# Performance work log

Hardware: AMD Instinct MI355X
Metric: run time of the kernel (lower is better)

The kernel has to match this reference:

```python
import jax, jax.numpy as jnp
import numpy as np

EPS = 1e-12


def setup_inputs() -> dict:
    key = jax.random.key(0)
    k1, k2 = jax.random.split(key)
    ide_feats = jax.random.normal(k1, (4096, 256), dtype=jnp.float32)
    u_feats = jax.random.normal(k2, (16384, 256), dtype=jnp.float32)
    return {"ide_feats": ide_feats, "u_feats": u_feats}


def reference(ide_feats, u_feats):
    # euclidean_dist: sqrt(sum((x_i - y_j)^2) + eps) -> [N, M]
    # computed via the GEMM expansion to avoid the [N, M, D] intermediate
    x2 = jnp.sum(ide_feats * ide_feats, axis=-1)[:, None]   # [N, 1]
    y2 = jnp.sum(u_feats * u_feats, axis=-1)[None, :]       # [1, M]
    xy = jnp.einsum('nd,md->nm', ide_feats, u_feats)        # [N, M]
    d2 = jnp.maximum(x2 + y2 - 2.0 * xy, 0.0)
    dists = jnp.sqrt(d2 + EPS)                              # [N, M]
    d = jnp.mean(dists, axis=-1)                            # [N]
    # dist_loss: sum_{i,j} sqrt((d_i - d_j)^2 + eps)
    diff = d[:, None] - d[None, :]                          # [N, N]
    loss = jnp.sum(jnp.sqrt(diff * diff + EPS))
    return loss
```

## Files before the change

kernel.cpp:

```cpp
#include <hip/hip_runtime.h>
#include <hip/hip_bf16.h>
#include <cstdint>

#define N_IDE 4096
#define M_U   16384
#define D_DIM 256
#define EPSF  1e-12f
#define INV_M (1.0f / 16384.0f)

typedef _Float16 f16x8 __attribute__((ext_vector_type(8)));
typedef float    f32x4 __attribute__((ext_vector_type(4)));

__device__ __forceinline__ void gll16(const void* g, void* l) {
  __builtin_amdgcn_global_load_lds(
      (const __attribute__((address_space(1))) void*)(uintptr_t)g,
      (__attribute__((address_space(3))) void*)(uint32_t)(uintptr_t)l,
      16, 0, 0);
}

__device__ __forceinline__ unsigned short f2h_bits(float f) {
  _Float16 h = (_Float16)f;
  return __builtin_bit_cast(unsigned short, h);
}

#define SBAR()  asm volatile("s_barrier" ::: "memory")

__global__ __launch_bounds__(256) void k_conv(const float* __restrict__ ide,
                                              const float* __restrict__ u,
                                              unsigned short* __restrict__ Ah,
                                              unsigned short* __restrict__ Bh,
                                              float* __restrict__ x2,
                                              float* __restrict__ y2) {
  int gw = (blockIdx.x * 256 + threadIdx.x) >> 6;
  int l  = threadIdx.x & 63;
  const float4* src;
  ushort4* dst;
  float* nrm;
  if (gw < N_IDE) {
    src = (const float4*)(ide + (size_t)gw * D_DIM);
    dst = (ushort4*)(Ah + (size_t)gw * D_DIM);
    nrm = x2 + gw;
  } else {
    int r = gw - N_IDE;
    src = (const float4*)(u + (size_t)r * D_DIM);
    dst = (ushort4*)(Bh + (size_t)r * D_DIM);
    nrm = y2 + r;
  }
  float4 v = src[l];
  float s = v.x * v.x + v.y * v.y + v.z * v.z + v.w * v.w;
  ushort4 o;
  o.x = f2h_bits(v.x); o.y = f2h_bits(v.y);
  o.z = f2h_bits(v.z); o.w = f2h_bits(v.w);
  dst[l] = o;
#pragma unroll
  for (int m = 1; m <= 32; m <<= 1) s += __shfl_xor(s, m, 64);
  if (l == 0) *nrm = s;
}

__global__ __launch_bounds__(512, 2) void k_gemm(const unsigned short* __restrict__ Ah,
                                                 const unsigned short* __restrict__ Bh,
                                                 const float* __restrict__ x2,
                                                 const float* __restrict__ y2,
                                                 float* __restrict__ partial) {
  __shared__ __align__(16) unsigned short sA[2][16384];
  __shared__ __align__(16) unsigned short sB[2][16384];
  __shared__ float rowacc[4][256];

  const int t    = threadIdx.x;
  const int w    = t >> 6;
  const int l    = t & 63;
  const int lrow = l & 15;
  const int lhi  = l >> 4;
  const int wm   = w >> 2, wn = w & 3;
  const int bn   = blockIdx.x;
  const int bm   = blockIdx.y;

  const int sr  = t >> 3;
  const int skc = (t & 7) ^ (sr & 7);
  const size_t soff = (size_t)sr * D_DIM + (size_t)skc * 8;

  const unsigned short* Abase = Ah + (size_t)bm * 256 * D_DIM;
  const unsigned short* Bbase = Bh + (size_t)bn * 256 * D_DIM;

  auto stA = [&](int k1, int h) {
    const unsigned short* src = Abase + (size_t)h * 128 * D_DIM + k1 * 64 + soff;
    unsigned short* dst = &sA[k1 & 1][h * 8192 + w * 512];
    gll16(src, dst);
    gll16(src + 64 * D_DIM, dst + 4096);
  };
  auto stB = [&](int k1, int h) {
    const unsigned short* src = Bbase + (size_t)h * 128 * D_DIM + k1 * 64 + soff;
    unsigned short* dst = &sB[k1 & 1][h * 8192 + w * 512];
    gll16(src, dst);
    gll16(src + 64 * D_DIM, dst + 4096);
  };

  stA(0, 0); stA(0, 1);
  stB(0, 0); stB(0, 1);
  stB(1, 0); stB(1, 1);
  asm volatile("s_waitcnt vmcnt(4)" ::: "memory");
  SBAR();

  const int sl0 = ((lhi)     ^ (lrow & 7)) * 8;
  const int sl1 = ((lhi + 4) ^ (lrow & 7)) * 8;

  f32x4 acc[8][4];
#pragma unroll
  for (int mi = 0; mi < 8; ++mi)
#pragma unroll
    for (int nj = 0; nj < 4; ++nj)
      acc[mi][nj] = (f32x4){0.f, 0.f, 0.f, 0.f};

#pragma unroll
  for (int kt = 0; kt < 4; ++kt) {
    const unsigned short* Ab = &sA[kt & 1][wm * 8192 + lrow * 64];
    const unsigned short* Bb = &sB[kt & 1][(wn >> 1) * 8192 + ((wn & 1) * 64 + lrow) * 64];
    f16x8 bf[4][2], af[4];

#pragma unroll
    for (int nj = 0; nj < 4; ++nj) {
      bf[nj][0] = *(const f16x8*)(Bb + nj * 1024 + sl0);
      bf[nj][1] = *(const f16x8*)(Bb + nj * 1024 + sl1);
    }
#pragma unroll
    for (int mi = 0; mi < 4; ++mi)
      af[mi] = *(const f16x8*)(Ab + mi * 1024 + sl0);
    if (kt < 3) stA(kt + 1, 0);
    SBAR();
    __builtin_amdgcn_s_setprio(1);
#pragma unroll
    for (int mi = 0; mi < 4; ++mi)
#pragma unroll
      for (int nj = 0; nj < 4; ++nj)
        acc[mi][nj] = __builtin_amdgcn_mfma_f32_16x16x32_f16(af[mi], bf[nj][0],
                                                             acc[mi][nj], 0, 0, 0);
    __builtin_amdgcn_s_setprio(0);
    SBAR();

#pragma unroll
    for (int mi = 0; mi < 4; ++mi)
      af[mi] = *(const f16x8*)(Ab + (64 + mi * 16) * 64 + sl0);
    if (kt < 3) stA(kt + 1, 1);
    SBAR();
    __builtin_amdgcn_s_setprio(1);
#pragma unroll
    for (int mi = 0; mi < 4; ++mi)
#pragma unroll
      for (int nj = 0; nj < 4; ++nj)
        acc[4 + mi][nj] = __builtin_amdgcn_mfma_f32_16x16x32_f16(af[mi], bf[nj][0],
                                                                 acc[4 + mi][nj], 0, 0, 0);
    __builtin_amdgcn_s_setprio(0);
    SBAR();

#pragma unroll
    for (int mi = 0; mi < 4; ++mi)
      af[mi] = *(const f16x8*)(Ab + mi * 1024 + sl1);
    if (kt < 2) stB(kt + 2, 0);
    SBAR();
    __builtin_amdgcn_s_setprio(1);
#pragma unroll
    for (int mi = 0; mi < 4; ++mi)
#pragma unroll
      for (int nj = 0; nj < 4; ++nj)
        acc[mi][nj] = __builtin_amdgcn_mfma_f32_16x16x32_f16(af[mi], bf[nj][1],
                                                             acc[mi][nj], 0, 0, 0);
    __builtin_amdgcn_s_setprio(0);
    SBAR();

#pragma unroll
    for (int mi = 0; mi < 4; ++mi)
      af[mi] = *(const f16x8*)(Ab + (64 + mi * 16) * 64 + sl1);
    if (kt < 2) stB(kt + 2, 1);
    SBAR();
    __builtin_amdgcn_s_setprio(1);
#pragma unroll
    for (int mi = 0; mi < 4; ++mi)
#pragma unroll
      for (int nj = 0; nj < 4; ++nj)
        acc[4 + mi][nj] = __builtin_amdgcn_mfma_f32_16x16x32_f16(af[mi], bf[nj][1],
                                                                 acc[4 + mi][nj], 0, 0, 0);
    __builtin_amdgcn_s_setprio(0);
    if (kt < 2)       asm volatile("s_waitcnt vmcnt(4)" ::: "memory");
    else if (kt == 2) asm volatile("s_waitcnt vmcnt(0)" ::: "memory");
    SBAR();
  }

  float yv[4];
#pragma unroll
  for (int nj = 0; nj < 4; ++nj)
    yv[nj] = y2[bn * 256 + wn * 64 + nj * 16 + lrow];

#pragma unroll
  for (int mi = 0; mi < 8; ++mi) {
    float4 x2v = *(const float4*)&x2[bm * 256 + wm * 128 + mi * 16 + lhi * 4];
    float xr[4] = {x2v.x, x2v.y, x2v.z, x2v.w};
    float rv[4];
#pragma unroll
    for (int rr = 0; rr < 4; ++rr) {
      float ssum = 0.f;
#pragma unroll
      for (int nj = 0; nj < 4; ++nj) {
        float d2 = xr[rr] + yv[nj] - 2.0f * acc[mi][nj][rr];
        d2 = fmaxf(d2, 0.0f);
        ssum += __builtin_amdgcn_sqrtf(d2 + EPSF);
      }
      ssum += __shfl_xor(ssum, 1, 64);
      ssum += __shfl_xor(ssum, 2, 64);
      ssum += __shfl_xor(ssum, 4, 64);
      ssum += __shfl_xor(ssum, 8, 64);
      rv[rr] = ssum;
    }
    if (lrow == 0)
      *(float4*)&rowacc[wn][wm * 128 + mi * 16 + lhi * 4] =
          make_float4(rv[0], rv[1], rv[2], rv[3]);
  }

  __syncthreads();
  if (t < 256)
    partial[(size_t)bn * N_IDE + bm * 256 + t] =
        rowacc[0][t] + rowacc[1][t] + rowacc[2][t] + rowacc[3][t];
}

__global__ __launch_bounds__(256) void k_dsum(const float* __restrict__ partial,
                                              float* __restrict__ d) {
  int k = blockIdx.x * 256 + threadIdx.x;
  float s = 0.f;
#pragma unroll
  for (int b = 0; b < 64; ++b) s += partial[(size_t)b * N_IDE + k];
  d[k] = s;
}

__global__ __launch_bounds__(256) void k_loss(const float* __restrict__ d,
                                              float* __restrict__ out) {
  __shared__ float sd[N_IDE];
  __shared__ float wsum[4];
  int t = threadIdx.x;
  for (int k = t; k < N_IDE; k += 256) sd[k] = d[k];
  __syncthreads();
  int tid = blockIdx.x * 256 + t;
  int i   = tid >> 4;
  int jl  = tid & 15;
  float di = sd[i];
  float s  = 0.f;
  for (int k = 0; k < 256; ++k) {
    float diff = (di - sd[jl + k * 16]) * INV_M;
    s += __builtin_amdgcn_sqrtf(diff * diff + EPSF);
  }
#pragma unroll
  for (int m = 1; m <= 32; m <<= 1) s += __shfl_xor(s, m, 64);
  if ((t & 63) == 0) wsum[t >> 6] = s;
  __syncthreads();
  if (t == 0) atomicAdd(out, wsum[0] + wsum[1] + wsum[2] + wsum[3]);
}

extern "C" void kernel_launch(void* const* d_in, const int* in_sizes, int n_in,
                              void* d_out, int out_size, void* d_ws, size_t ws_size,
                              hipStream_t stream) {
  (void)in_sizes; (void)n_in; (void)out_size; (void)ws_size;
  const float* ide = (const float*)d_in[0];
  const float* u   = (const float*)d_in[1];
  float* out = (float*)d_out;

  char* ws = (char*)d_ws;
  size_t off = 0;
  unsigned short* Ah = (unsigned short*)(ws + off); off += (size_t)N_IDE * D_DIM * 2;
  unsigned short* Bh = (unsigned short*)(ws + off); off += (size_t)M_U  * D_DIM * 2;
  float* x2      = (float*)(ws + off); off += (size_t)N_IDE * 4;
  float* y2      = (float*)(ws + off); off += (size_t)M_U * 4;
  float* partial = (float*)(ws + off); off += (size_t)64 * N_IDE * 4;
  float* dvec    = (float*)(ws + off); off += (size_t)N_IDE * 4;

  hipMemsetAsync(d_out, 0, sizeof(float), stream);
  k_conv<<<(N_IDE + M_U) / 4, 256, 0, stream>>>(ide, u, Ah, Bh, x2, y2);
  k_gemm<<<dim3(64, 16), 512, 0, stream>>>(Ah, Bh, x2, y2, partial);
  k_dsum<<<N_IDE / 256, 256, 0, stream>>>(partial, dvec);
  k_loss<<<256, 256, 0, stream>>>(dvec, out);
}
```

Before: 152.0 us.

## Restructure GEMM K-loop pipeline, fold dsum into loss, drop memset

The GEMM main loop is reorganized so that LDS fragments for the next k-tile are register-prefetched while MFMAs run, and the next tile's A and B global-to-LDS loads are issued together once per k-tile instead of staggered two tiles ahead for B. Separately, the d-vector reduction kernel is removed: each k_loss block now sums the 64 partials itself. The hipMemsetAsync of the output is replaced by a store inside k_conv. These changes cut launches and barriers, but every loss block now redundantly reads the full partial buffer, and the shallower B prefetch may expose more load latency.

```diff
diff --git a/kernel.cpp b/kernel.cpp
--- a/kernel.cpp
+++ b/kernel.cpp
@@ -30,7 +30,9 @@
                                               unsigned short* __restrict__ Ah,
                                               unsigned short* __restrict__ Bh,
                                               float* __restrict__ x2,
-                                              float* __restrict__ y2) {
+                                              float* __restrict__ y2,
+                                              float* __restrict__ out) {
+  if (blockIdx.x == 0 && threadIdx.x == 0) out[0] = 0.f;
   int gw = (blockIdx.x * 256 + threadIdx.x) >> 6;
   int l  = threadIdx.x & 63;
   const float4* src;
@@ -97,12 +99,23 @@
 
   stA(0, 0); stA(0, 1);
   stB(0, 0); stB(0, 1);
-  stB(1, 0); stB(1, 1);
-  asm volatile("s_waitcnt vmcnt(4)" ::: "memory");
+  asm volatile("s_waitcnt vmcnt(0)" ::: "memory");
   SBAR();
 
   const int sl0 = ((lhi)     ^ (lrow & 7)) * 8;
   const int sl1 = ((lhi + 4) ^ (lrow & 7)) * 8;
+
+  f16x8 afA[4], afB[4], bf0[4], bf1[4];
+  {
+    const unsigned short* Ab0 = &sA[0][wm * 8192 + lrow * 64];
+    const unsigned short* Bb0 = &sB[0][(wn >> 1) * 8192 + ((wn & 1) * 64 + lrow) * 64];
+#pragma unroll
+    for (int nj = 0; nj < 4; ++nj)
+      bf0[nj] = *(const f16x8*)(Bb0 + nj * 1024 + sl0);
+#pragma unroll
+    for (int mi = 0; mi < 4; ++mi)
+      afA[mi] = *(const f16x8*)(Ab0 + mi * 1024 + sl0);
+  }
 
   f32x4 acc[8][4];
 #pragma unroll
@@ -115,73 +128,69 @@
   for (int kt = 0; kt < 4; ++kt) {
     const unsigned short* Ab = &sA[kt & 1][wm * 8192 + lrow * 64];
     const unsigned short* Bb = &sB[kt & 1][(wn >> 1) * 8192 + ((wn & 1) * 64 + lrow) * 64];
-    f16x8 bf[4][2], af[4];
-
-#pragma unroll
-    for (int nj = 0; nj < 4; ++nj) {
-      bf[nj][0] = *(const f16x8*)(Bb + nj * 1024 + sl0);
-      bf[nj][1] = *(const f16x8*)(Bb + nj * 1024 + sl1);
+
+    __builtin_amdgcn_s_setprio(1);
+#pragma unroll
+    for (int mi = 0; mi < 4; ++mi)
+#pragma unroll
+      for (int nj = 0; nj < 4; ++nj)
+        acc[mi][nj] = __builtin_amdgcn_mfma_f32_16x16x32_f16(afA[mi], bf0[nj],
+                                                             acc[mi][nj], 0, 0, 0);
+    __builtin_amdgcn_s_setprio(0);
+#pragma unroll
+    for (int mi = 0; mi < 4; ++mi)
+      afB[mi] = *(const f16x8*)(Ab + (64 + mi * 16) * 64 + sl0);
+    if (kt < 3) { stA(kt + 1, 0); stA(kt + 1, 1); stB(kt + 1, 0); stB(kt + 1, 1); }
+    SBAR();
+
+    __builtin_amdgcn_s_setprio(1);
+#pragma unroll
+    for (int mi = 0; mi < 4; ++mi)
+#pragma unroll
+      for (int nj = 0; nj < 4; ++nj)
+        acc[4 + mi][nj] = __builtin_amdgcn_mfma_f32_16x16x32_f16(afB[mi], bf0[nj],
+                                                                 acc[4 + mi][nj], 0, 0, 0);
+    __builtin_amdgcn_s_setprio(0);
+#pragma unroll
+    for (int mi = 0; mi < 4; ++mi)
+      afA[mi] = *(const f16x8*)(Ab + mi * 1024 + sl1);
+#pragma unroll
+    for (int nj = 0; nj < 4; ++nj)
+      bf1[nj] = *(const f16x8*)(Bb + nj * 1024 + sl1);
+    SBAR();
+
+    __builtin_amdgcn_s_setprio(1);
+#pragma unroll
+    for (int mi = 0; mi < 4; ++mi)
+#pragma unroll
+      for (int nj = 0; nj < 4; ++nj)
+        acc[mi][nj] = __builtin_amdgcn_mfma_f32_16x16x32_f16(afA[mi], bf1[nj],
+                                                             acc[mi][nj], 0, 0, 0);
+    __builtin_amdgcn_s_setprio(0);
+#pragma unroll
+    for (int mi = 0; mi < 4; ++mi)
+      afB[mi] = *(const f16x8*)(Ab + (64 + mi * 16) * 64 + sl1);
+    if (kt < 3) asm volatile("s_waitcnt vmcnt(0)" ::: "memory");
+    SBAR();
+
+    __builtin_amdgcn_s_setprio(1);
+#pragma unroll
+    for (int mi = 0; mi < 4; ++mi)
+#pragma unroll
+      for (int nj = 0; nj < 4; ++nj)
+        acc[4 + mi][nj] = __builtin_amdgcn_mfma_f32_16x16x32_f16(afB[mi], bf1[nj],
+                                                                 acc[4 + mi][nj], 0, 0, 0);
+    __builtin_amdgcn_s_setprio(0);
+    if (kt < 3) {
+      const unsigned short* Abn = &sA[(kt + 1) & 1][wm * 8192 + lrow * 64];
+      const unsigned short* Bbn = &sB[(kt + 1) & 1][(wn >> 1) * 8192 + ((wn & 1) * 64 + lrow) * 64];
+#pragma unroll
+      for (int nj = 0; nj < 4; ++nj)
+        bf0[nj] = *(const f16x8*)(Bbn + nj * 1024 + sl0);
+#pragma unroll
+      for (int mi = 0; mi < 4; ++mi)
+        afA[mi] = *(const f16x8*)(Abn + mi * 1024 + sl0);
     }
-#pragma unroll
-    for (int mi = 0; mi < 4; ++mi)
-      af[mi] = *(const f16x8*)(Ab + mi * 1024 + sl0);
-    if (kt < 3) stA(kt + 1, 0);
-    SBAR();
-    __builtin_amdgcn_s_setprio(1);
-#pragma unroll
-    for (int mi = 0; mi < 4; ++mi)
-#pragma unroll
-      for (int nj = 0; nj < 4; ++nj)
-        acc[mi][nj] = __builtin_amdgcn_mfma_f32_16x16x32_f16(af[mi], bf[nj][0],
-                                                             acc[mi][nj], 0, 0, 0);
-    __builtin_amdgcn_s_setprio(0);
-    SBAR();
-
-#pragma unroll
-    for (int mi = 0; mi < 4; ++mi)
-      af[mi] = *(const f16x8*)(Ab + (64 + mi * 16) * 64 + sl0);
-    if (kt < 3) stA(kt + 1, 1);
-    SBAR();
-    __builtin_amdgcn_s_setprio(1);
-#pragma unroll
-    for (int mi = 0; mi < 4; ++mi)
-#pragma unroll
-      for (int nj = 0; nj < 4; ++nj)
-        acc[4 + mi][nj] = __builtin_amdgcn_mfma_f32_16x16x32_f16(af[mi], bf[nj][0],
-                                                                 acc[4 + mi][nj], 0, 0, 0);
-    __builtin_amdgcn_s_setprio(0);
-    SBAR();
-
-#pragma unroll
-    for (int mi = 0; mi < 4; ++mi)
-      af[mi] = *(const f16x8*)(Ab + mi * 1024 + sl1);
-    if (kt < 2) stB(kt + 2, 0);
-    SBAR();
-    __builtin_amdgcn_s_setprio(1);
-#pragma unroll
-    for (int mi = 0; mi < 4; ++mi)
-#pragma unroll
-      for (int nj = 0; nj < 4; ++nj)
-        acc[mi][nj] = __builtin_amdgcn_mfma_f32_16x16x32_f16(af[mi], bf[nj][1],
-                                                             acc[mi][nj], 0, 0, 0);
-    __builtin_amdgcn_s_setprio(0);
-    SBAR();
-
-#pragma unroll
-    for (int mi = 0; mi < 4; ++mi)
-      af[mi] = *(const f16x8*)(Ab + (64 + mi * 16) * 64 + sl1);
-    if (kt < 2) stB(kt + 2, 1);
-    SBAR();
-    __builtin_amdgcn_s_setprio(1);
-#pragma unroll
-    for (int mi = 0; mi < 4; ++mi)
-#pragma unroll
-      for (int nj = 0; nj < 4; ++nj)
-        acc[4 + mi][nj] = __builtin_amdgcn_mfma_f32_16x16x32_f16(af[mi], bf[nj][1],
-                                                                 acc[4 + mi][nj], 0, 0, 0);
-    __builtin_amdgcn_s_setprio(0);
-    if (kt < 2)       asm volatile("s_waitcnt vmcnt(4)" ::: "memory");
-    else if (kt == 2) asm volatile("s_waitcnt vmcnt(0)" ::: "memory");
     SBAR();
   }
 
@@ -221,21 +230,17 @@
         rowacc[0][t] + rowacc[1][t] + rowacc[2][t] + rowacc[3][t];
 }
 
-__global__ __launch_bounds__(256) void k_dsum(const float* __restrict__ partial,
-                                              float* __restrict__ d) {
-  int k = blockIdx.x * 256 + threadIdx.x;
-  float s = 0.f;
-#pragma unroll
-  for (int b = 0; b < 64; ++b) s += partial[(size_t)b * N_IDE + k];
-  d[k] = s;
-}
-
-__global__ __launch_bounds__(256) void k_loss(const float* __restrict__ d,
+__global__ __launch_bounds__(256) void k_loss(const float* __restrict__ partial,
                                               float* __restrict__ out) {
   __shared__ float sd[N_IDE];
   __shared__ float wsum[4];
   int t = threadIdx.x;
-  for (int k = t; k < N_IDE; k += 256) sd[k] = d[k];
+  for (int k = t; k < N_IDE; k += 256) {
+    float s = 0.f;
+#pragma unroll
+    for (int b = 0; b < 64; ++b) s += partial[(size_t)b * N_IDE + k];
+    sd[k] = s;
+  }
   __syncthreads();
   int tid = blockIdx.x * 256 + t;
   int i   = tid >> 4;
@@ -268,11 +273,8 @@
   float* x2      = (float*)(ws + off); off += (size_t)N_IDE * 4;
   float* y2      = (float*)(ws + off); off += (size_t)M_U * 4;
   float* partial = (float*)(ws + off); off += (size_t)64 * N_IDE * 4;
-  float* dvec    = (float*)(ws + off); off += (size_t)N_IDE * 4;
-
-  hipMemsetAsync(d_out, 0, sizeof(float), stream);
-  k_conv<<<(N_IDE + M_U) / 4, 256, 0, stream>>>(ide, u, Ah, Bh, x2, y2);
+
+  k_conv<<<(N_IDE + M_U) / 4, 256, 0, stream>>>(ide, u, Ah, Bh, x2, y2, out);
   k_gemm<<<dim3(64, 16), 512, 0, stream>>>(Ah, Bh, x2, y2, partial);
-  k_dsum<<<N_IDE / 256, 256, 0, stream>>>(partial, dvec);
-  k_loss<<<256, 256, 0, stream>>>(dvec, out);
-}
+  k_loss<<<256, 256, 0, stream>>>(partial, out);
+}
```

Result: slower. 250.2 us (+64.6%).
